# Kernel optimization log

Measured on AMD Instinct MI355X. Metric: run time of the kernel, lower is better.

The kernel has to match this reference:

```python
import jax, jax.numpy as jnp
import numpy as np

LAYERS, STACKS = 10, 4
DILATIONS = [2 ** l for _ in range(STACKS) for l in range(LAYERS)]  # 40 blocks


def setup_inputs() -> dict:
    key = jax.random.key(0)
    ks = jax.random.split(key, 7)
    B, C, L, SC, NB = 4, 64, 8192, 256, len(DILATIONS)
    scale = 0.05  # keep 40 stacked residual blocks numerically tame
    return {
        "x": jax.random.normal(ks[0], (B, C, L), dtype=jnp.float32),
        "dc_w": jax.random.normal(ks[1], (NB, C, C, 2), dtype=jnp.float32) * scale,
        "dc_b": jax.random.normal(ks[2], (NB, C), dtype=jnp.float32) * scale,
        "conv_w": jax.random.normal(ks[3], (NB, C, C), dtype=jnp.float32) * scale,
        "conv_b": jax.random.normal(ks[4], (NB, C), dtype=jnp.float32) * scale,
        "skip_w": jax.random.normal(ks[5], (NB, SC, C), dtype=jnp.float32) * scale,
        "skip_b": jax.random.normal(ks[6], (NB, SC), dtype=jnp.float32) * scale,
        "skip_size": 4096,
    }


def reference(x, dc_w, dc_b, conv_w, conv_b, skip_w, skip_b, skip_size):
    # x: [B, res_ch, L]; returns stacked skips [n_blocks, B, skip_ch, skip_size]
    out = x
    skips = []
    for i, d in enumerate(DILATIONS):
        h = (jnp.einsum('oi,bil->bol', dc_w[i, :, :, 0], out[:, :, :-d])
             + jnp.einsum('oi,bil->bol', dc_w[i, :, :, 1], out[:, :, d:])
             + dc_b[i][None, :, None])
        g = jax.nn.relu(h)
        r = jnp.einsum('oi,bil->bol', conv_w[i], g) + conv_b[i][None, :, None]
        out = r + out[:, :, -r.shape[2]:]  # residual on aligned (last) timesteps
        s = jnp.einsum('oi,bil->bol', skip_w[i], g) + skip_b[i][None, :, None]
        skips.append(s[:, :, -skip_size:])
    return jnp.stack(skips)
```

## Files before the change

### kernel.cpp

```cpp
#include <hip/hip_runtime.h>


#define CC    64
#define SCC   256
#define BB    4
#define LL0   8192
#define NBLK  40
#define SKIPN 4096
#define TTC   32

typedef __attribute__((ext_vector_type(8))) short bf16x8;
typedef __attribute__((ext_vector_type(4))) float f32x4;
typedef unsigned short us;

__device__ __forceinline__ us f2bf(float f) {
    union { float f; unsigned u; } v; v.f = f;
    return (us)((v.u + 0x7FFF + ((v.u >> 16) & 1)) >> 16);
}
__device__ __forceinline__ unsigned pk2(float a, float b) {
    return (unsigned)f2bf(a) | ((unsigned)f2bf(b) << 16);
}
__device__ __forceinline__ uint2 pk4(f32x4 v) {
    return (uint2){pk2(v[0], v[1]), pk2(v[2], v[3])};
}
__device__ __forceinline__ bf16x8 pack8(f32x4 u0, f32x4 u1) {
    bf16x8 r;
    r[0]=(short)f2bf(u0[0]); r[1]=(short)f2bf(u0[1]);
    r[2]=(short)f2bf(u0[2]); r[3]=(short)f2bf(u0[3]);
    r[4]=(short)f2bf(u1[0]); r[5]=(short)f2bf(u1[1]);
    r[6]=(short)f2bf(u1[2]); r[7]=(short)f2bf(u1[3]);
    return r;
}
__device__ __forceinline__ int sws(int r, int c) {
    return (r << 6) + ((((c >> 3) ^ r) & 7) << 3) + (c & 7);
}
__device__ __forceinline__ int swh(int r, int c) {
    return (r << 6) + ((((c >> 3) ^ r) & 7) << 3) + (c & 7);
}
__device__ __forceinline__ int swx(int r, int k) {
    int ch = k >> 3; ch = (ch & 8) | ((ch ^ r) & 7);
    return (r << 7) + (ch << 3) + (k & 7);
}

__global__ __launch_bounds__(256) void prep_kernel(
    const float* __restrict__ x, float* __restrict__ xt_out,
    const float* __restrict__ dc_w, const float* __restrict__ conv_w,
    const float* __restrict__ skip_w,
    us* __restrict__ wcat, us* __restrict__ cwb, us* __restrict__ swb)
{
    if (blockIdx.x < 512) {
        __shared__ float tile[64][65];
        const int b = blockIdx.x >> 7, t0 = (blockIdx.x & 127) * 64;
        const int tid = threadIdx.x;
        #pragma unroll
        for (int p = 0; p < 4; ++p) {
            const int c = p * 16 + (tid >> 4), j = tid & 15;
            const float4 v = *(const float4*)(x + ((size_t)b * CC + c) * LL0 + t0 + j * 4);
            tile[c][j*4+0]=v.x; tile[c][j*4+1]=v.y; tile[c][j*4+2]=v.z; tile[c][j*4+3]=v.w;
        }
        __syncthreads();
        #pragma unroll
        for (int p = 0; p < 4; ++p) {
            const int r = p * 16 + (tid >> 4), h = tid & 15;
            float4 v = {tile[h*4+0][r], tile[h*4+1][r], tile[h*4+2][r], tile[h*4+3][r]};
            *(float4*)(xt_out + ((size_t)b * LL0 + t0 + r) * CC + h * 4) = v;
        }
        return;
    }
    const int n_sw = NBLK * SCC * CC, n_cw = NBLK * CC * CC, n_wc = NBLK * CC * 128;
    for (int idx = (blockIdx.x - 512) * blockDim.x + threadIdx.x; idx < n_sw;
         idx += 1024 * blockDim.x) {
        swb[idx] = f2bf(skip_w[idx]);
        if (idx < n_cw) cwb[idx] = f2bf(conv_w[idx]);
        if (idx < n_wc) {
            const int i = idx >> 13, o = (idx >> 7) & 63, kk = idx & 127;
            wcat[idx] = f2bf(dc_w[(((i * CC + o) * CC) + (kk & 63)) * 2 + (kk >> 6)]);
        }
    }
}

template<int NW>
__device__ __forceinline__ void skip_body(
    int e, int blk0,
    const us* __restrict__ g_all, const us* __restrict__ swb,
    const float* __restrict__ skip_b, float* __restrict__ out)
{
    constexpr int ROWS = NW * 16;
    constexpr int TPB = (SKIPN / ROWS) * BB;
    const int tid = threadIdx.x, lane = tid & 63, wv = tid >> 6;
    const int j = blk0 + e / TPB;
    const int id = e % TPB;
    const int tt = id % (SKIPN / ROWS);
    const int b  = id / (SKIPN / ROWS);
    const us* g  = g_all + ((size_t)j * BB + b) * SKIPN * CC;
    const us* sw = swb + (size_t)j * SCC * CC;
    const float* sb = skip_b + j * SCC;
    float* op = out + ((size_t)j * BB + b) * SCC * SKIPN;

    const int trow = tt * ROWS + wv * 16 + (lane & 15);
    bf16x8 a[2];
    a[0] = *(const bf16x8*)(g + (size_t)trow * CC + (lane >> 4) * 8);
    a[1] = *(const bf16x8*)(g + (size_t)trow * CC + 32 + (lane >> 4) * 8);
    const int tstore = tt * ROWS + wv * 16 + ((lane >> 4) << 2);
    #pragma unroll 4
    for (int n = 0; n < 16; ++n) {
        const int sc = n * 16 + (lane & 15);
        const float bias = sb[sc];
        f32x4 acc = (f32x4){bias, bias, bias, bias};
        const us* wrow = sw + sc * CC + (lane >> 4) * 8;
        acc = __builtin_amdgcn_mfma_f32_16x16x32_bf16(a[0], *(const bf16x8*)(wrow), acc, 0, 0, 0);
        acc = __builtin_amdgcn_mfma_f32_16x16x32_bf16(a[1], *(const bf16x8*)(wrow + 32), acc, 0, 0, 0);
        *(float4*)(op + (size_t)sc * SKIPN + tstore) = (float4){acc[0], acc[1], acc[2], acc[3]};
    }
}

template<int NB, int DB, int TOUT, int RCAP, int MAXCH>
__global__ __launch_bounds__(512) void fused_kernel(
    const float* __restrict__ cur, float* __restrict__ nxt,
    const us* __restrict__ wcat_all, const us* __restrict__ cwb_all,
    const float* __restrict__ db_all, const float* __restrict__ cb_all,
    us* __restrict__ g_all, int blk0, int Lin, int ntiles,
    const us* __restrict__ swb, const float* __restrict__ skip_b,
    float* __restrict__ out, int pb0)
{
    const int wg = blockIdx.x, chain = BB * ntiles;
    if (wg >= chain) { skip_body<8>(wg - chain, pb0, g_all, swb, skip_b, out); return; }

    constexpr int H  = DB * ((1 << NB) - 1);
    constexpr int R0 = TOUT + H;
    __shared__ __align__(16) float sm[RCAP * CC];
    __shared__ __align__(16) us  gsm[RCAP * CC];

    const int tid = threadIdx.x, lane = tid & 63, wv = tid >> 6;
    const int b = wg / ntiles, t0 = (wg % ntiles) * TOUT;
    const float* src = cur + (size_t)b * LL0 * CC;

    for (int base = 0; base < R0; base += 32) {
        const int row = base + (tid >> 4);
        const int h4 = (tid & 15) * 4;
        if (row < R0) {
            int gt = t0 + row; if (gt > Lin - 1) gt = Lin - 1;
            *(f32x4*)(sm + sws(row, h4)) = *(const f32x4*)(src + (size_t)gt * CC + h4);
        }
    }
    __syncthreads();

    const int rf = wv >> 1, oh = wv & 1;
    const int c8 = (lane >> 4) * 8;
    int Rcur = R0, Lj = Lin;

    for (int j = 0; j < NB; ++j) {
        const int d = DB << j;
        const int Rn = Rcur - d;
        Lj -= d;
        const us* wj = wcat_all + (size_t)(blk0 + j) * CC * 128;
        const us* cj = cwb_all + (size_t)(blk0 + j) * CC * CC;
        const float* dbj = db_all + (blk0 + j) * CC;
        const float* cbj = cb_all + (blk0 + j) * CC;

        #pragma unroll
        for (int ch = 0; ch < MAXCH; ++ch) {
            if (ch * 64 < Rn) {
                const int t = ch * 64 + rf * 16 + (lane & 15);
                const int tc = t > Rn - 1 ? Rn - 1 : t;
                bf16x8 af[4];
                af[0] = pack8(*(const f32x4*)(sm + sws(tc, c8)),
                              *(const f32x4*)(sm + sws(tc, c8 + 4)));
                af[1] = pack8(*(const f32x4*)(sm + sws(tc, 32 + c8)),
                              *(const f32x4*)(sm + sws(tc, 36 + c8)));
                af[2] = pack8(*(const f32x4*)(sm + sws(tc + d, c8)),
                              *(const f32x4*)(sm + sws(tc + d, c8 + 4)));
                af[3] = pack8(*(const f32x4*)(sm + sws(tc + d, 32 + c8)),
                              *(const f32x4*)(sm + sws(tc + d, 36 + c8)));
                #pragma unroll
                for (int n = 0; n < 2; ++n) {
                    const int orow = oh * 32 + n * 16 + (lane & 15);
                    const int o0   = oh * 32 + n * 16 + (lane >> 4) * 4;
                    f32x4 acc = *(const f32x4*)(dbj + o0);
                    const us* wr = wj + orow * 128 + c8;
                    acc = __builtin_amdgcn_mfma_f32_16x16x32_bf16(*(const bf16x8*)(wr),      af[0], acc, 0, 0, 0);
                    acc = __builtin_amdgcn_mfma_f32_16x16x32_bf16(*(const bf16x8*)(wr + 32), af[1], acc, 0, 0, 0);
                    acc = __builtin_amdgcn_mfma_f32_16x16x32_bf16(*(const bf16x8*)(wr + 64), af[2], acc, 0, 0, 0);
                    acc = __builtin_amdgcn_mfma_f32_16x16x32_bf16(*(const bf16x8*)(wr + 96), af[3], acc, 0, 0, 0);
                    #pragma unroll
                    for (int r = 0; r < 4; ++r) acc[r] = acc[r] > 0.f ? acc[r] : 0.f;
                    if (t < Rn) *(uint2*)(gsm + swh(t, o0)) = pk4(acc);
                }
            }
        }
        __syncthreads();

        f32x4 oldv[MAXCH][2];
        #pragma unroll
        for (int ch = 0; ch < MAXCH; ++ch) {
            if (ch * 64 < Rn) {
                const int t = ch * 64 + rf * 16 + (lane & 15);
                const int tc = t > Rn - 1 ? Rn - 1 : t;
                #pragma unroll
                for (int n = 0; n < 2; ++n) {
                    const int o0 = oh * 32 + n * 16 + (lane >> 4) * 4;
                    oldv[ch][n] = *(const f32x4*)(sm + sws(tc + d, o0));
                }
            }
        }
        {
            const int wbase = Lj - SKIPN;
            us* gdst = g_all + ((size_t)(blk0 + j) * BB + b) * SKIPN * CC;
            const int ch8 = tid & 7;
            for (int grow = tid >> 3; grow < Rn; grow += 64) {
                const int gt = t0 + grow;
                if (gt < Lj && gt >= wbase)
                    *(bf16x8*)(gdst + ((size_t)(gt - wbase)) * CC + ch8 * 8) =
                        *(const bf16x8*)(gsm + swh(grow, ch8 * 8));
            }
        }
        __syncthreads();

        #pragma unroll
        for (int ch = 0; ch < MAXCH; ++ch) {
            if (ch * 64 < Rn) {
                const int t = ch * 64 + rf * 16 + (lane & 15);
                const int tc = t > Rn - 1 ? Rn - 1 : t;
                bf16x8 g0 = *(const bf16x8*)(gsm + swh(tc, c8));
                bf16x8 g1 = *(const bf16x8*)(gsm + swh(tc, 32 + c8));
                #pragma unroll
                for (int n = 0; n < 2; ++n) {
                    const int orow = oh * 32 + n * 16 + (lane & 15);
                    const int o0   = oh * 32 + n * 16 + (lane >> 4) * 4;
                    f32x4 r = *(const f32x4*)(cbj + o0);
                    const us* wr = cj + orow * 64 + c8;
                    r = __builtin_amdgcn_mfma_f32_16x16x32_bf16(*(const bf16x8*)(wr),      g0, r, 0, 0, 0);
                    r = __builtin_amdgcn_mfma_f32_16x16x32_bf16(*(const bf16x8*)(wr + 32), g1, r, 0, 0, 0);
                    r += oldv[ch][n];
                    if (t < Rn) *(f32x4*)(sm + sws(t, o0)) = r;
                }
            }
        }
        __syncthreads();
        Rcur = Rn;
    }

    float* dst = nxt + (size_t)b * LL0 * CC;
    for (int base = 0; base < TOUT; base += 32) {
        const int row = base + (tid >> 4);
        const int h4 = (tid & 15) * 4;
        const int gt = t0 + row;
        if (row < TOUT && gt < Lj)
            *(float4*)(dst + (size_t)gt * CC + h4) = *(const float4*)(sm + sws(row, h4));
    }
}

__global__ __launch_bounds__(256) void block_kernel(
    const float* __restrict__ cur, float* __restrict__ nxt,
    const us* __restrict__ wcat, const us* __restrict__ cwb,
    const float* __restrict__ db, const float* __restrict__ cb,
    us* __restrict__ g_out,
    int d, int Lin, int Lout, int ntiles,
    const us* __restrict__ g_all, const us* __restrict__ swb,
    const float* __restrict__ skip_b, float* __restrict__ out, int pb0)
{
    const int wg = blockIdx.x, chain = BB * ntiles;
    if (wg >= chain) { skip_body<4>(wg - chain, pb0, g_all, swb, skip_b, out); return; }

    __shared__ __align__(16) us xt[TTC * 128];
    __shared__ __align__(16) us gs[TTC * CC];
    __shared__ __align__(16) float x1f[TTC * CC];
    __shared__ __align__(16) float rs[TTC * CC];

    const int tid = threadIdx.x, lane = tid & 63, wv = tid >> 6;
    const int b = wg / ntiles, t0 = (wg % ntiles) * TTC;
    const float* src = cur + (size_t)b * LL0 * CC;

    #pragma unroll
    for (int p = 0; p < 2; ++p) {
        const int row = p * 16 + (tid >> 4);
        const int h4 = (tid & 15) * 4;
        int ta = t0 + row;     if (ta > Lin - 1) ta = Lin - 1;
        int tb = t0 + row + d; if (tb > Lin - 1) tb = Lin - 1;
        f32x4 v0 = *(const f32x4*)(src + (size_t)ta * CC + h4);
        f32x4 v1 = *(const f32x4*)(src + (size_t)tb * CC + h4);
        *(uint2*)(xt + swx(row, h4))      = pk4(v0);
        *(uint2*)(xt + swx(row, 64 + h4)) = pk4(v1);
        *(f32x4*)(x1f + sws(row, h4)) = v1;
    }
    __syncthreads();

    const int rf = wv >> 1, oh = wv & 1;
    const int t = rf * 16 + (lane & 15);
    const int c8 = (lane >> 4) * 8;

    bf16x8 af[4];
    #pragma unroll
    for (int ks = 0; ks < 4; ++ks)
        af[ks] = *(const bf16x8*)(xt + swx(t, ks * 32 + c8));
    #pragma unroll
    for (int n = 0; n < 2; ++n) {
        const int orow = oh * 32 + n * 16 + (lane & 15);
        const int o0   = oh * 32 + n * 16 + (lane >> 4) * 4;
        f32x4 acc = *(const f32x4*)(db + o0);
        const us* wr = wcat + orow * 128 + c8;
        acc = __builtin_amdgcn_mfma_f32_16x16x32_bf16(*(const bf16x8*)(wr),      af[0], acc, 0, 0, 0);
        acc = __builtin_amdgcn_mfma_f32_16x16x32_bf16(*(const bf16x8*)(wr + 32), af[1], acc, 0, 0, 0);
        acc = __builtin_amdgcn_mfma_f32_16x16x32_bf16(*(const bf16x8*)(wr + 64), af[2], acc, 0, 0, 0);
        acc = __builtin_amdgcn_mfma_f32_16x16x32_bf16(*(const bf16x8*)(wr + 96), af[3], acc, 0, 0, 0);
        #pragma unroll
        for (int r = 0; r < 4; ++r) acc[r] = acc[r] > 0.f ? acc[r] : 0.f;
        *(uint2*)(gs + swh(t, o0)) = pk4(acc);
    }
    __syncthreads();

    bf16x8 g0 = *(const bf16x8*)(gs + swh(t, c8));
    bf16x8 g1 = *(const bf16x8*)(gs + swh(t, 32 + c8));
    #pragma unroll
    for (int n = 0; n < 2; ++n) {
        const int orow = oh * 32 + n * 16 + (lane & 15);
        const int o0   = oh * 32 + n * 16 + (lane >> 4) * 4;
        f32x4 r = *(const f32x4*)(cb + o0);
        const us* wr = cwb + orow * 64 + c8;
        r = __builtin_amdgcn_mfma_f32_16x16x32_bf16(*(const bf16x8*)(wr),      g0, r, 0, 0, 0);
        r = __builtin_amdgcn_mfma_f32_16x16x32_bf16(*(const bf16x8*)(wr + 32), g1, r, 0, 0, 0);
        r += *(const f32x4*)(x1f + sws(t, o0));
        *(f32x4*)(rs + sws(t, o0)) = r;
    }
    __syncthreads();

    #pragma unroll
    for (int p = 0; p < 2; ++p) {
        const int row = p * 16 + (tid >> 4);
        const int h4 = (tid & 15) * 4;
        const int gt = t0 + row;
        if (gt < Lout)
            *(float4*)(nxt + (size_t)b * LL0 * CC + (size_t)gt * CC + h4) =
                *(const float4*)(rs + sws(row, h4));
    }
    {
        const int row = tid >> 3, ch8 = tid & 7;
        const int gt = t0 + row;
        const int wbase = Lout - SKIPN;
        if (gt >= wbase && gt < Lout)
            *(bf16x8*)(g_out + ((size_t)b * SKIPN + (gt - wbase)) * CC + ch8 * 8) =
                *(const bf16x8*)(gs + swh(row, ch8 * 8));
    }
}

__global__ __launch_bounds__(256) void skip_kernel(
    const us* __restrict__ g_all, const us* __restrict__ swb,
    const float* __restrict__ skip_b, float* __restrict__ out, int blk0)
{
    skip_body<4>(blockIdx.x, blk0, g_all, swb, skip_b, out);
}

extern "C" void kernel_launch(void* const* d_in, const int* in_sizes, int n_in,
                              void* d_out, int out_size, void* d_ws, size_t ws_size,
                              hipStream_t stream)
{
    const float* x      = (const float*)d_in[0];
    const float* dc_w   = (const float*)d_in[1];
    const float* dc_b   = (const float*)d_in[2];
    const float* conv_w = (const float*)d_in[3];
    const float* conv_b = (const float*)d_in[4];
    const float* skip_w = (const float*)d_in[5];
    const float* skip_b = (const float*)d_in[6];
    float* out = (float*)d_out;

    char* ws = (char*)d_ws;
    float* bufA = (float*)ws;  ws += (size_t)BB * LL0 * CC * 4;
    float* bufB = (float*)ws;  ws += (size_t)BB * LL0 * CC * 4;
    us* g_all = (us*)ws;       ws += (size_t)NBLK * BB * SKIPN * CC * 2;
    us* wcat  = (us*)ws;       ws += (size_t)NBLK * CC * 128 * 2;
    us* cwb   = (us*)ws;       ws += (size_t)NBLK * CC * CC * 2;
    us* swb   = (us*)ws;       ws += (size_t)NBLK * SCC * CC * 2;

    prep_kernel<<<1536, 256, 0, stream>>>(x, bufA, dc_w, conv_w, skip_w, wcat, cwb, swb);

    float* bufs[2] = {bufA, bufB};
    int Lc = LL0, blk = 0, q = 0, produced = 0, skipped = 0;
    for (int s = 0; s < 4; ++s) {
        {
            const int Lout = Lc - 63;
            const int nt = (Lout + 95) / 96;
            int cap = produced - skipped; if (cap > 3) cap = 3;
            const int grid = BB * nt + cap * 128;
            fused_kernel<6, 1, 96, 160, 3><<<dim3(grid), 512, 0, stream>>>(
                bufs[q & 1], bufs[(q + 1) & 1], wcat, cwb, dc_b, conv_b,
                g_all, blk, Lc, nt, swb, skip_b, out, skipped);
            skipped += cap; produced += 6; blk += 6; Lc = Lout; ++q;
        }
        for (int dl = 6; dl < 10; ++dl) {
            const int d = 1 << dl;
            const int Lout = Lc - d;
            const int nt = (Lout + TTC - 1) / TTC;
            int cap = produced - skipped; if (cap > 3) cap = 3;
            const int grid = BB * nt + cap * 256;
            block_kernel<<<dim3(grid), 256, 0, stream>>>(
                bufs[q & 1], bufs[(q + 1) & 1],
                wcat + (size_t)blk * CC * 128, cwb + (size_t)blk * CC * CC,
                dc_b + blk * CC, conv_b + blk * CC,
                g_all + (size_t)blk * BB * SKIPN * CC,
                d, Lc, Lout, nt, g_all, swb, skip_b, out, skipped);
            skipped += cap; produced += 1; blk += 1; Lc = Lout; ++q;
        }
    }
    const int rem = NBLK - skipped;
    if (rem > 0)
        skip_kernel<<<dim3(rem * 256), 256, 0, stream>>>(g_all, swb, skip_b, out, skipped);
}
```

Baseline: 760.5 us.

## Fuse dilation-64/128 and 256/512 block pairs into single kernels, wave-local gate scratch

Replaces the four per-block launches for dilations 64..512 with two pair kernels that each compute two consecutive residual blocks, recomputing the intermediate residual for the needed time offsets inside one workgroup. This removes two global write/read round-trips of the full activation buffer per stack and two launches. The fused 6-layer kernel is restructured so each wave owns whole 16-row fragments across all 64 output channels, keeping the gate in a per-wave LDS scratch, which drops one barrier per layer and writes skip activations directly. The skip-kernel cap also rises from 3 to 4 per launch. The cost is redundant computation of the first block of each pair for overlapping rows, plus larger LDS use.

```diff
diff --git a/kernel.cpp b/kernel.cpp
--- a/kernel.cpp
+++ b/kernel.cpp
@@ -7,7 +7,6 @@
 #define LL0   8192
 #define NBLK  40
 #define SKIPN 4096
-#define TTC   32
 
 typedef __attribute__((ext_vector_type(8))) short bf16x8;
 typedef __attribute__((ext_vector_type(4))) float f32x4;
@@ -34,12 +33,8 @@
 __device__ __forceinline__ int sws(int r, int c) {
     return (r << 6) + ((((c >> 3) ^ r) & 7) << 3) + (c & 7);
 }
-__device__ __forceinline__ int swh(int r, int c) {
-    return (r << 6) + ((((c >> 3) ^ r) & 7) << 3) + (c & 7);
-}
-__device__ __forceinline__ int swx(int r, int k) {
-    int ch = k >> 3; ch = (ch & 8) | ((ch ^ r) & 7);
-    return (r << 7) + (ch << 3) + (k & 7);
+__device__ __forceinline__ int scb(int s, int chunk) {
+    return (s << 6) + (((chunk ^ (s & 7)) & 7) << 3);
 }
 
 __global__ __launch_bounds__(256) void prep_kernel(
@@ -114,8 +109,7 @@
     }
 }
 
-template<int NB, int DB, int TOUT, int RCAP, int MAXCH>
-__global__ __launch_bounds__(512) void fused_kernel(
+__global__ __launch_bounds__(512) void fused6_kernel(
     const float* __restrict__ cur, float* __restrict__ nxt,
     const us* __restrict__ wcat_all, const us* __restrict__ cwb_all,
     const float* __restrict__ db_all, const float* __restrict__ cb_all,
@@ -126,14 +120,15 @@
     const int wg = blockIdx.x, chain = BB * ntiles;
     if (wg >= chain) { skip_body<8>(wg - chain, pb0, g_all, swb, skip_b, out); return; }
 
-    constexpr int H  = DB * ((1 << NB) - 1);
-    constexpr int R0 = TOUT + H;
+    constexpr int TOUT = 96, R0 = 159, RCAP = 160;
     __shared__ __align__(16) float sm[RCAP * CC];
-    __shared__ __align__(16) us  gsm[RCAP * CC];
+    __shared__ __align__(16) us  scr[8 * 16 * CC];
 
     const int tid = threadIdx.x, lane = tid & 63, wv = tid >> 6;
     const int b = wg / ntiles, t0 = (wg % ntiles) * TOUT;
     const float* src = cur + (size_t)b * LL0 * CC;
+    const int s = lane & 15, q = lane >> 4;
+    us* myscr = scr + wv * (16 * CC);
 
     for (int base = 0; base < R0; base += 32) {
         const int row = base + (tid >> 4);
@@ -145,95 +140,81 @@
     }
     __syncthreads();
 
-    const int rf = wv >> 1, oh = wv & 1;
-    const int c8 = (lane >> 4) * 8;
     int Rcur = R0, Lj = Lin;
-
-    for (int j = 0; j < NB; ++j) {
-        const int d = DB << j;
+    for (int j = 0; j < 6; ++j) {
+        const int d = 1 << j;
         const int Rn = Rcur - d;
         Lj -= d;
         const us* wj = wcat_all + (size_t)(blk0 + j) * CC * 128;
         const us* cj = cwb_all + (size_t)(blk0 + j) * CC * CC;
         const float* dbj = db_all + (blk0 + j) * CC;
         const float* cbj = cb_all + (blk0 + j) * CC;
-
-        #pragma unroll
-        for (int ch = 0; ch < MAXCH; ++ch) {
-            if (ch * 64 < Rn) {
-                const int t = ch * 64 + rf * 16 + (lane & 15);
+        const int wbase = Lj - SKIPN;
+        us* gdst = g_all + ((size_t)(blk0 + j) * BB + b) * SKIPN * CC;
+
+        f32x4 r2[2][4];
+        #pragma unroll
+        for (int fi = 0; fi < 2; ++fi) {
+            const int fg = wv + fi * 8;
+            const bool act = fg * 16 < Rn;
+            if (act) {
+                const int t = fg * 16 + s;
                 const int tc = t > Rn - 1 ? Rn - 1 : t;
-                bf16x8 af[4];
-                af[0] = pack8(*(const f32x4*)(sm + sws(tc, c8)),
-                              *(const f32x4*)(sm + sws(tc, c8 + 4)));
-                af[1] = pack8(*(const f32x4*)(sm + sws(tc, 32 + c8)),
-                              *(const f32x4*)(sm + sws(tc, 36 + c8)));
-                af[2] = pack8(*(const f32x4*)(sm + sws(tc + d, c8)),
-                              *(const f32x4*)(sm + sws(tc + d, c8 + 4)));
-                af[3] = pack8(*(const f32x4*)(sm + sws(tc + d, 32 + c8)),
-                              *(const f32x4*)(sm + sws(tc + d, 36 + c8)));
+                bf16x8 af0 = pack8(*(const f32x4*)(sm + sws(tc, q * 8)),
+                                   *(const f32x4*)(sm + sws(tc, q * 8 + 4)));
+                bf16x8 af1 = pack8(*(const f32x4*)(sm + sws(tc, 32 + q * 8)),
+                                   *(const f32x4*)(sm + sws(tc, 36 + q * 8)));
+                bf16x8 af2 = pack8(*(const f32x4*)(sm + sws(tc + d, q * 8)),
+                                   *(const f32x4*)(sm + sws(tc + d, q * 8 + 4)));
+                bf16x8 af3 = pack8(*(const f32x4*)(sm + sws(tc + d, 32 + q * 8)),
+                                   *(const f32x4*)(sm + sws(tc + d, 36 + q * 8)));
                 #pragma unroll
-                for (int n = 0; n < 2; ++n) {
-                    const int orow = oh * 32 + n * 16 + (lane & 15);
-                    const int o0   = oh * 32 + n * 16 + (lane >> 4) * 4;
+                for (int n = 0; n < 4; ++n) {
+                    const int o0 = n * 16 + q * 4;
                     f32x4 acc = *(const f32x4*)(dbj + o0);
-                    const us* wr = wj + orow * 128 + c8;
-                    acc = __builtin_amdgcn_mfma_f32_16x16x32_bf16(*(const bf16x8*)(wr),      af[0], acc, 0, 0, 0);
-                    acc = __builtin_amdgcn_mfma_f32_16x16x32_bf16(*(const bf16x8*)(wr + 32), af[1], acc, 0, 0, 0);
-                    acc = __builtin_amdgcn_mfma_f32_16x16x32_bf16(*(const bf16x8*)(wr + 64), af[2], acc, 0, 0, 0);
-                    acc = __builtin_amdgcn_mfma_f32_16x16x32_bf16(*(const bf16x8*)(wr + 96), af[3], acc, 0, 0, 0);
+                    const us* wr = wj + (n * 16 + s) * 128 + q * 8;
+                    acc = __builtin_amdgcn_mfma_f32_16x16x32_bf16(*(const bf16x8*)(wr),      af0, acc, 0, 0, 0);
+                    acc = __builtin_amdgcn_mfma_f32_16x16x32_bf16(*(const bf16x8*)(wr + 32), af1, acc, 0, 0, 0);
+                    acc = __builtin_amdgcn_mfma_f32_16x16x32_bf16(*(const bf16x8*)(wr + 64), af2, acc, 0, 0, 0);
+                    acc = __builtin_amdgcn_mfma_f32_16x16x32_bf16(*(const bf16x8*)(wr + 96), af3, acc, 0, 0, 0);
                     #pragma unroll
                     for (int r = 0; r < 4; ++r) acc[r] = acc[r] > 0.f ? acc[r] : 0.f;
-                    if (t < Rn) *(uint2*)(gsm + swh(t, o0)) = pk4(acc);
+                    *(uint2*)(myscr + scb(s, n * 2 + (q >> 1)) + (q & 1) * 4) = pk4(acc);
+                }
+                {
+                    const int gt = t0 + t;
+                    if (t < Rn && gt >= wbase && gt < Lj) {
+                        us* gr = gdst + (size_t)(gt - wbase) * CC;
+                        #pragma unroll
+                        for (int h = 0; h < 2; ++h) {
+                            const int ck = q * 2 + h;
+                            *(bf16x8*)(gr + ck * 8) = *(const bf16x8*)(myscr + scb(s, ck));
+                        }
+                    }
+                }
+                bf16x8 g0 = *(const bf16x8*)(myscr + scb(s, q));
+                bf16x8 g1 = *(const bf16x8*)(myscr + scb(s, 4 + q));
+                #pragma unroll
+                for (int n = 0; n < 4; ++n) {
+                    const int o0 = n * 16 + q * 4;
+                    f32x4 r = *(const f32x4*)(cbj + o0);
+                    const us* wr = cj + (n * 16 + s) * CC + q * 8;
+                    r = __builtin_amdgcn_mfma_f32_16x16x32_bf16(*(const bf16x8*)(wr),      g0, r, 0, 0, 0);
+                    r = __builtin_amdgcn_mfma_f32_16x16x32_bf16(*(const bf16x8*)(wr + 32), g1, r, 0, 0, 0);
+                    r += *(const f32x4*)(sm + sws(tc + d, o0));
+                    r2[fi][n] = r;
                 }
             }
         }
         __syncthreads();
-
-        f32x4 oldv[MAXCH][2];
-        #pragma unroll
-        for (int ch = 0; ch < MAXCH; ++ch) {
-            if (ch * 64 < Rn) {
-                const int t = ch * 64 + rf * 16 + (lane & 15);
-                const int tc = t > Rn - 1 ? Rn - 1 : t;
+        #pragma unroll
+        for (int fi = 0; fi < 2; ++fi) {
+            const int fg = wv + fi * 8;
+            const int t = fg * 16 + s;
+            if (t < Rn) {
                 #pragma unroll
-                for (int n = 0; n < 2; ++n) {
-                    const int o0 = oh * 32 + n * 16 + (lane >> 4) * 4;
-                    oldv[ch][n] = *(const f32x4*)(sm + sws(tc + d, o0));
-                }
-            }
-        }
-        {
-            const int wbase = Lj - SKIPN;
-            us* gdst = g_all + ((size_t)(blk0 + j) * BB + b) * SKIPN * CC;
-            const int ch8 = tid & 7;
-            for (int grow = tid >> 3; grow < Rn; grow += 64) {
-                const int gt = t0 + grow;
-                if (gt < Lj && gt >= wbase)
-                    *(bf16x8*)(gdst + ((size_t)(gt - wbase)) * CC + ch8 * 8) =
-                        *(const bf16x8*)(gsm + swh(grow, ch8 * 8));
-            }
-        }
-        __syncthreads();
-
-        #pragma unroll
-        for (int ch = 0; ch < MAXCH; ++ch) {
-            if (ch * 64 < Rn) {
-                const int t = ch * 64 + rf * 16 + (lane & 15);
-                const int tc = t > Rn - 1 ? Rn - 1 : t;
-                bf16x8 g0 = *(const bf16x8*)(gsm + swh(tc, c8));
-                bf16x8 g1 = *(const bf16x8*)(gsm + swh(tc, 32 + c8));
-                #pragma unroll
-                for (int n = 0; n < 2; ++n) {
-                    const int orow = oh * 32 + n * 16 + (lane & 15);
-                    const int o0   = oh * 32 + n * 16 + (lane >> 4) * 4;
-                    f32x4 r = *(const f32x4*)(cbj + o0);
-                    const us* wr = cj + orow * 64 + c8;
-                    r = __builtin_amdgcn_mfma_f32_16x16x32_bf16(*(const bf16x8*)(wr),      g0, r, 0, 0, 0);
-                    r = __builtin_amdgcn_mfma_f32_16x16x32_bf16(*(const bf16x8*)(wr + 32), g1, r, 0, 0, 0);
-                    r += oldv[ch][n];
-                    if (t < Rn) *(f32x4*)(sm + sws(t, o0)) = r;
-                }
+                for (int n = 0; n < 4; ++n)
+                    *(f32x4*)(sm + sws(t, n * 16 + q * 4)) = r2[fi][n];
             }
         }
         __syncthreads();
@@ -250,96 +231,148 @@
     }
 }
 
-__global__ __launch_bounds__(256) void block_kernel(
+template<int D>
+__global__ __launch_bounds__(256) void pair_kernel(
     const float* __restrict__ cur, float* __restrict__ nxt,
-    const us* __restrict__ wcat, const us* __restrict__ cwb,
-    const float* __restrict__ db, const float* __restrict__ cb,
-    us* __restrict__ g_out,
-    int d, int Lin, int Lout, int ntiles,
+    const us* __restrict__ wA, const us* __restrict__ wB,
+    const us* __restrict__ cA, const us* __restrict__ cB,
+    const float* __restrict__ dbA, const float* __restrict__ dbB,
+    const float* __restrict__ cbA, const float* __restrict__ cbB,
+    us* __restrict__ gA_out, us* __restrict__ gB_out,
+    int Lin, int ntB,
     const us* __restrict__ g_all, const us* __restrict__ swb,
     const float* __restrict__ skip_b, float* __restrict__ out, int pb0)
 {
-    const int wg = blockIdx.x, chain = BB * ntiles;
+    const int wg = blockIdx.x, chain = BB * ntB;
     if (wg >= chain) { skip_body<4>(wg - chain, pb0, g_all, swb, skip_b, out); return; }
 
-    __shared__ __align__(16) us xt[TTC * 128];
-    __shared__ __align__(16) us gs[TTC * CC];
-    __shared__ __align__(16) float x1f[TTC * CC];
-    __shared__ __align__(16) float rs[TTC * CC];
+    __shared__ __align__(16) float xs[4 * 32 * CC];
+    __shared__ __align__(16) float ms[2 * 32 * CC];
+    __shared__ __align__(16) us  scr[4 * 16 * CC];
 
     const int tid = threadIdx.x, lane = tid & 63, wv = tid >> 6;
-    const int b = wg / ntiles, t0 = (wg % ntiles) * TTC;
+    const int b = wg / ntB, T0 = (wg % ntB) * 32;
     const float* src = cur + (size_t)b * LL0 * CC;
+    const int s = lane & 15, q = lane >> 4;
+    us* myscr = scr + wv * (16 * CC);
+    const int LoutA = Lin - D, Lout2 = Lin - 3 * D;
 
     #pragma unroll
-    for (int p = 0; p < 2; ++p) {
+    for (int p = 0; p < 8; ++p) {
         const int row = p * 16 + (tid >> 4);
+        const int st = row >> 5, r = row & 31;
         const int h4 = (tid & 15) * 4;
-        int ta = t0 + row;     if (ta > Lin - 1) ta = Lin - 1;
-        int tb = t0 + row + d; if (tb > Lin - 1) tb = Lin - 1;
-        f32x4 v0 = *(const f32x4*)(src + (size_t)ta * CC + h4);
-        f32x4 v1 = *(const f32x4*)(src + (size_t)tb * CC + h4);
-        *(uint2*)(xt + swx(row, h4))      = pk4(v0);
-        *(uint2*)(xt + swx(row, 64 + h4)) = pk4(v1);
-        *(f32x4*)(x1f + sws(row, h4)) = v1;
+        int gt = T0 + st * D + r; if (gt > Lin - 1) gt = Lin - 1;
+        *(f32x4*)(xs + st * (32 * CC) + sws(r, h4)) =
+            *(const f32x4*)(src + (size_t)gt * CC + h4);
     }
     __syncthreads();
 
-    const int rf = wv >> 1, oh = wv & 1;
-    const int t = rf * 16 + (lane & 15);
-    const int c8 = (lane >> 4) * 8;
-
-    bf16x8 af[4];
-    #pragma unroll
-    for (int ks = 0; ks < 4; ++ks)
-        af[ks] = *(const bf16x8*)(xt + swx(t, ks * 32 + c8));
-    #pragma unroll
-    for (int n = 0; n < 2; ++n) {
-        const int orow = oh * 32 + n * 16 + (lane & 15);
-        const int o0   = oh * 32 + n * 16 + (lane >> 4) * 4;
-        f32x4 acc = *(const f32x4*)(db + o0);
-        const us* wr = wcat + orow * 128 + c8;
-        acc = __builtin_amdgcn_mfma_f32_16x16x32_bf16(*(const bf16x8*)(wr),      af[0], acc, 0, 0, 0);
-        acc = __builtin_amdgcn_mfma_f32_16x16x32_bf16(*(const bf16x8*)(wr + 32), af[1], acc, 0, 0, 0);
-        acc = __builtin_amdgcn_mfma_f32_16x16x32_bf16(*(const bf16x8*)(wr + 64), af[2], acc, 0, 0, 0);
-        acc = __builtin_amdgcn_mfma_f32_16x16x32_bf16(*(const bf16x8*)(wr + 96), af[3], acc, 0, 0, 0);
-        #pragma unroll
-        for (int r = 0; r < 4; ++r) acc[r] = acc[r] > 0.f ? acc[r] : 0.f;
-        *(uint2*)(gs + swh(t, o0)) = pk4(acc);
+    {
+        const int m = wv >> 1, rA = (wv & 1) * 16 + s;
+        const int tA = T0 + m * 2 * D + rA;
+        const float* x0 = xs + (2 * m) * (32 * CC);
+        const float* x1 = xs + (2 * m + 1) * (32 * CC);
+        bf16x8 af0 = pack8(*(const f32x4*)(x0 + sws(rA, q * 8)),
+                           *(const f32x4*)(x0 + sws(rA, q * 8 + 4)));
+        bf16x8 af1 = pack8(*(const f32x4*)(x0 + sws(rA, 32 + q * 8)),
+                           *(const f32x4*)(x0 + sws(rA, 36 + q * 8)));
+        bf16x8 af2 = pack8(*(const f32x4*)(x1 + sws(rA, q * 8)),
+                           *(const f32x4*)(x1 + sws(rA, q * 8 + 4)));
+        bf16x8 af3 = pack8(*(const f32x4*)(x1 + sws(rA, 32 + q * 8)),
+                           *(const f32x4*)(x1 + sws(rA, 36 + q * 8)));
+        #pragma unroll
+        for (int n = 0; n < 4; ++n) {
+            const int o0 = n * 16 + q * 4;
+            f32x4 acc = *(const f32x4*)(dbA + o0);
+            const us* wr = wA + (n * 16 + s) * 128 + q * 8;
+            acc = __builtin_amdgcn_mfma_f32_16x16x32_bf16(*(const bf16x8*)(wr),      af0, acc, 0, 0, 0);
+            acc = __builtin_amdgcn_mfma_f32_16x16x32_bf16(*(const bf16x8*)(wr + 32), af1, acc, 0, 0, 0);
+            acc = __builtin_amdgcn_mfma_f32_16x16x32_bf16(*(const bf16x8*)(wr + 64), af2, acc, 0, 0, 0);
+            acc = __builtin_amdgcn_mfma_f32_16x16x32_bf16(*(const bf16x8*)(wr + 96), af3, acc, 0, 0, 0);
+            #pragma unroll
+            for (int r = 0; r < 4; ++r) acc[r] = acc[r] > 0.f ? acc[r] : 0.f;
+            *(uint2*)(myscr + scb(s, n * 2 + (q >> 1)) + (q & 1) * 4) = pk4(acc);
+        }
+        {
+            const int wbA = LoutA - SKIPN;
+            const bool own = (m == 0) || (tA >= ntB * 32);
+            if (own && tA >= wbA && tA < LoutA) {
+                us* gr = gA_out + ((size_t)b * SKIPN + (tA - wbA)) * CC;
+                #pragma unroll
+                for (int h = 0; h < 2; ++h) {
+                    const int ck = q * 2 + h;
+                    *(bf16x8*)(gr + ck * 8) = *(const bf16x8*)(myscr + scb(s, ck));
+                }
+            }
+        }
+        bf16x8 g0 = *(const bf16x8*)(myscr + scb(s, q));
+        bf16x8 g1 = *(const bf16x8*)(myscr + scb(s, 4 + q));
+        #pragma unroll
+        for (int n = 0; n < 4; ++n) {
+            const int o0 = n * 16 + q * 4;
+            f32x4 r = *(const f32x4*)(cbA + o0);
+            const us* wr = cA + (n * 16 + s) * CC + q * 8;
+            r = __builtin_amdgcn_mfma_f32_16x16x32_bf16(*(const bf16x8*)(wr),      g0, r, 0, 0, 0);
+            r = __builtin_amdgcn_mfma_f32_16x16x32_bf16(*(const bf16x8*)(wr + 32), g1, r, 0, 0, 0);
+            r += *(const f32x4*)(x1 + sws(rA, o0));
+            *(f32x4*)(ms + m * (32 * CC) + sws(rA, o0)) = r;
+        }
     }
     __syncthreads();
 
-    bf16x8 g0 = *(const bf16x8*)(gs + swh(t, c8));
-    bf16x8 g1 = *(const bf16x8*)(gs + swh(t, 32 + c8));
-    #pragma unroll
-    for (int n = 0; n < 2; ++n) {
-        const int orow = oh * 32 + n * 16 + (lane & 15);
-        const int o0   = oh * 32 + n * 16 + (lane >> 4) * 4;
-        f32x4 r = *(const f32x4*)(cb + o0);
-        const us* wr = cwb + orow * 64 + c8;
-        r = __builtin_amdgcn_mfma_f32_16x16x32_bf16(*(const bf16x8*)(wr),      g0, r, 0, 0, 0);
-        r = __builtin_amdgcn_mfma_f32_16x16x32_bf16(*(const bf16x8*)(wr + 32), g1, r, 0, 0, 0);
-        r += *(const f32x4*)(x1f + sws(t, o0));
-        *(f32x4*)(rs + sws(t, o0)) = r;
-    }
-    __syncthreads();
-
-    #pragma unroll
-    for (int p = 0; p < 2; ++p) {
-        const int row = p * 16 + (tid >> 4);
-        const int h4 = (tid & 15) * 4;
-        const int gt = t0 + row;
-        if (gt < Lout)
-            *(float4*)(nxt + (size_t)b * LL0 * CC + (size_t)gt * CC + h4) =
-                *(const float4*)(rs + sws(row, h4));
-    }
     {
-        const int row = tid >> 3, ch8 = tid & 7;
-        const int gt = t0 + row;
-        const int wbase = Lout - SKIPN;
-        if (gt >= wbase && gt < Lout)
-            *(bf16x8*)(g_out + ((size_t)b * SKIPN + (gt - wbase)) * CC + ch8 * 8) =
-                *(const bf16x8*)(gs + swh(row, ch8 * 8));
+        const int rB = (wv & 1) * 16 + s;
+        const int tB = T0 + rB;
+        const bool lead = wv < 2;
+        const float* m0 = ms;
+        const float* m1 = ms + 32 * CC;
+        bf16x8 af0 = pack8(*(const f32x4*)(m0 + sws(rB, q * 8)),
+                           *(const f32x4*)(m0 + sws(rB, q * 8 + 4)));
+        bf16x8 af1 = pack8(*(const f32x4*)(m0 + sws(rB, 32 + q * 8)),
+                           *(const f32x4*)(m0 + sws(rB, 36 + q * 8)));
+        bf16x8 af2 = pack8(*(const f32x4*)(m1 + sws(rB, q * 8)),
+                           *(const f32x4*)(m1 + sws(rB, q * 8 + 4)));
+        bf16x8 af3 = pack8(*(const f32x4*)(m1 + sws(rB, 32 + q * 8)),
+                           *(const f32x4*)(m1 + sws(rB, 36 + q * 8)));
+        #pragma unroll
+        for (int n = 0; n < 4; ++n) {
+            const int o0 = n * 16 + q * 4;
+            f32x4 acc = *(const f32x4*)(dbB + o0);
+            const us* wr = wB + (n * 16 + s) * 128 + q * 8;
+            acc = __builtin_amdgcn_mfma_f32_16x16x32_bf16(*(const bf16x8*)(wr),      af0, acc, 0, 0, 0);
+            acc = __builtin_amdgcn_mfma_f32_16x16x32_bf16(*(const bf16x8*)(wr + 32), af1, acc, 0, 0, 0);
+            acc = __builtin_amdgcn_mfma_f32_16x16x32_bf16(*(const bf16x8*)(wr + 64), af2, acc, 0, 0, 0);
+            acc = __builtin_amdgcn_mfma_f32_16x16x32_bf16(*(const bf16x8*)(wr + 96), af3, acc, 0, 0, 0);
+            #pragma unroll
+            for (int r = 0; r < 4; ++r) acc[r] = acc[r] > 0.f ? acc[r] : 0.f;
+            *(uint2*)(myscr + scb(s, n * 2 + (q >> 1)) + (q & 1) * 4) = pk4(acc);
+        }
+        {
+            const int wbB = Lout2 - SKIPN;
+            if (lead && tB >= wbB && tB < Lout2) {
+                us* gr = gB_out + ((size_t)b * SKIPN + (tB - wbB)) * CC;
+                #pragma unroll
+                for (int h = 0; h < 2; ++h) {
+                    const int ck = q * 2 + h;
+                    *(bf16x8*)(gr + ck * 8) = *(const bf16x8*)(myscr + scb(s, ck));
+                }
+            }
+        }
+        bf16x8 g0 = *(const bf16x8*)(myscr + scb(s, q));
+        bf16x8 g1 = *(const bf16x8*)(myscr + scb(s, 4 + q));
+        float* dst = nxt + (size_t)b * LL0 * CC;
+        #pragma unroll
+        for (int n = 0; n < 4; ++n) {
+            const int o0 = n * 16 + q * 4;
+            f32x4 r = *(const f32x4*)(cbB + o0);
+            const us* wr = cB + (n * 16 + s) * CC + q * 8;
+            r = __builtin_amdgcn_mfma_f32_16x16x32_bf16(*(const bf16x8*)(wr),      g0, r, 0, 0, 0);
+            r = __builtin_amdgcn_mfma_f32_16x16x32_bf16(*(const bf16x8*)(wr + 32), g1, r, 0, 0, 0);
+            r += *(const f32x4*)(m1 + sws(rB, o0));
+            if (lead && tB < Lout2)
+                *(f32x4*)(dst + (size_t)tB * CC + o0) = r;
+        }
     }
 }
 
@@ -374,31 +407,44 @@
     prep_kernel<<<1536, 256, 0, stream>>>(x, bufA, dc_w, conv_w, skip_w, wcat, cwb, swb);
 
     float* bufs[2] = {bufA, bufB};
+    const size_t GSZ = (size_t)BB * SKIPN * CC;
     int Lc = LL0, blk = 0, q = 0, produced = 0, skipped = 0;
-    for (int s = 0; s < 4; ++s) {
+    for (int st = 0; st < 4; ++st) {
         {
             const int Lout = Lc - 63;
             const int nt = (Lout + 95) / 96;
-            int cap = produced - skipped; if (cap > 3) cap = 3;
-            const int grid = BB * nt + cap * 128;
-            fused_kernel<6, 1, 96, 160, 3><<<dim3(grid), 512, 0, stream>>>(
+            int cap = produced - skipped; if (cap > 4) cap = 4;
+            fused6_kernel<<<dim3(BB * nt + cap * 128), 512, 0, stream>>>(
                 bufs[q & 1], bufs[(q + 1) & 1], wcat, cwb, dc_b, conv_b,
                 g_all, blk, Lc, nt, swb, skip_b, out, skipped);
             skipped += cap; produced += 6; blk += 6; Lc = Lout; ++q;
         }
-        for (int dl = 6; dl < 10; ++dl) {
-            const int d = 1 << dl;
-            const int Lout = Lc - d;
-            const int nt = (Lout + TTC - 1) / TTC;
-            int cap = produced - skipped; if (cap > 3) cap = 3;
+        #pragma unroll
+        for (int pi = 0; pi < 2; ++pi) {
+            const int D = pi == 0 ? 64 : 256;
+            const int Lout2 = Lc - 3 * D;
+            const int nt = (Lout2 + 31) / 32;
+            int cap = produced - skipped; if (cap > 4) cap = 4;
             const int grid = BB * nt + cap * 256;
-            block_kernel<<<dim3(grid), 256, 0, stream>>>(
-                bufs[q & 1], bufs[(q + 1) & 1],
-                wcat + (size_t)blk * CC * 128, cwb + (size_t)blk * CC * CC,
-                dc_b + blk * CC, conv_b + blk * CC,
-                g_all + (size_t)blk * BB * SKIPN * CC,
-                d, Lc, Lout, nt, g_all, swb, skip_b, out, skipped);
-            skipped += cap; produced += 1; blk += 1; Lc = Lout; ++q;
+            if (D == 64)
+                pair_kernel<64><<<dim3(grid), 256, 0, stream>>>(
+                    bufs[q & 1], bufs[(q + 1) & 1],
+                    wcat + (size_t)blk * CC * 128, wcat + (size_t)(blk + 1) * CC * 128,
+                    cwb + (size_t)blk * CC * CC, cwb + (size_t)(blk + 1) * CC * CC,
+                    dc_b + blk * CC, dc_b + (blk + 1) * CC,
+                    conv_b + blk * CC, conv_b + (blk + 1) * CC,
+                    g_all + (size_t)blk * GSZ, g_all + (size_t)(blk + 1) * GSZ,
+                    Lc, nt, g_all, swb, skip_b, out, skipped);
+            else
+                pair_kernel<256><<<dim3(grid), 256, 0, stream>>>(
+                    bufs[q & 1], bufs[(q + 1) & 1],
+                    wcat + (size_t)blk * CC * 128, wcat + (size_t)(blk + 1) * CC * 128,
+                    cwb + (size_t)blk * CC * CC, cwb + (size_t)(blk + 1) * CC * CC,
+                    dc_b + blk * CC, dc_b + (blk + 1) * CC,
+                    conv_b + blk * CC, conv_b + (blk + 1) * CC,
+                    g_all + (size_t)blk * GSZ, g_all + (size_t)(blk + 1) * GSZ,
+                    Lc, nt, g_all, swb, skip_b, out, skipped);
+            skipped += cap; produced += 2; blk += 2; Lc = Lout2; ++q;
         }
     }
     const int rem = NBLK - skipped;
```

Result: no change. 770.5 us (+1.3%).
